# Performance work log

Hardware: AMD Instinct MI355X
Metric: run time of the kernel (lower is better)

The kernel has to match this reference:

```python
import jax, jax.numpy as jnp
import numpy as np

C_IN = 32
C_OUT = 32


def setup_inputs() -> dict:
    key = jax.random.key(0)
    k1, k2, k3 = jax.random.split(key, 3)
    B, N, P_DIM = 32, 4096, 64
    X = jax.random.normal(k1, (B, N, C_IN), dtype=jnp.float32)
    P = jax.random.normal(k2, (B, N, P_DIM), dtype=jnp.float32)
    # glorot-ish scale for the hypernetwork Dense kernel (p_dim -> c_in*c_out)
    scale = (2.0 / (P_DIM + C_IN * C_OUT)) ** 0.5
    Wk = jax.random.normal(k3, (P_DIM, C_IN * C_OUT), dtype=jnp.float32) * scale
    return {"X": X, "P": P, "Wk": Wk}


def reference(X, P, Wk):
    B, N, c_in = X.shape
    # hypernetwork: per-position weight generation  [B,N,p] @ [p, c_in*c_out]
    A = jnp.einsum('bnp,pq->bnq', P, Wk)
    W = A.reshape(B, N, c_in, C_OUT)          # [B,N,c_in,c_out]
    W = jax.nn.relu(W)                        # sigma(W)
    # batched per-position GEMV: y_bno = sum_i X_bni * W_bnio
    out = jnp.einsum('bni,bnio->bno', X, W)   # [B,N,c_out]
    return out
```

## Files before the change

kernel.cpp:

```cpp
#include <hip/hip_runtime.h>

#define CI 32
#define CO 32
#define PD 64
#define QDIM 1024
#define M_TOTAL (32*4096)
#define TILE_M 256
#define NBLK (M_TOTAL/TILE_M)
#define WG_THREADS 256

typedef float  f32x4  __attribute__((ext_vector_type(4)));
typedef float  f32x16 __attribute__((ext_vector_type(16)));
typedef __bf16 bf16x4 __attribute__((ext_vector_type(4)));
typedef __bf16 bf16x8 __attribute__((ext_vector_type(8)));

#define XLS 257
#define OLS 33

__global__ __launch_bounds__(256)
void wk_pack_kernel(const float* __restrict__ Wk, __bf16* __restrict__ wsF)
{
    __shared__ float tile[64][33];
    const int q0 = blockIdx.x * 32;
    const int t  = threadIdx.x;
#pragma unroll
    for (int s = 0; s < 2; ++s) {
        const int idx = t + s * 256;
        const int k = idx >> 3, ch = idx & 7;
        f32x4 v = *(const f32x4*)(Wk + (size_t)k * QDIM + q0 + ch * 4);
        tile[k][ch*4+0] = v[0]; tile[k][ch*4+1] = v[1];
        tile[k][ch*4+2] = v[2]; tile[k][ch*4+3] = v[3];
    }
    __syncthreads();
    const int qq = t >> 3;
    const int g  = t & 7;
    bf16x8 o;
#pragma unroll
    for (int j = 0; j < 8; ++j) o[j] = (__bf16)tile[g*8 + j][qq];
    *(bf16x8*)(wsF + (size_t)blockIdx.x * 2048 + g * 256 + qq * 8) = o;
}

__global__ __launch_bounds__(WG_THREADS, 2)
void cond_dense_kernel(const float* __restrict__ Xg, const float* __restrict__ Pg,
                       const __bf16* __restrict__ wsF, float* __restrict__ outg)
{
    __shared__ union {
        __bf16 p[TILE_M * PD];
        float  o[TILE_M * OLS];
    } U;
    __shared__ float Xl[CI * XLS];

    const int tid = threadIdx.x;
    const int l   = tid & 63;
    const int w   = tid >> 6;
    const int l31 = l & 31;
    const int hi  = l >> 5;
    const int mlo = w * 64 + l31;
    const int mhi = mlo + 32;
    const int tile0 = blockIdx.x * TILE_M;

    {
        const float* Pb = Pg + (size_t)tile0 * PD;
        const int pr = tid >> 4, pch = tid & 15;
#pragma unroll
        for (int s = 0; s < 16; ++s) {
            const int r = pr + s * 16;
            f32x4 v = *(const f32x4*)(Pb + (size_t)r * PD + pch * 4);
            bf16x4 bv;
#pragma unroll
            for (int j = 0; j < 4; ++j) bv[j] = (__bf16)v[j];
            char* dst = (char*)U.p + r * 128
                      + ((((pch >> 1) ^ (r & 7)) << 4) | ((pch & 1) * 8));
            *(bf16x4*)dst = bv;
        }
        const float* Xb = Xg + (size_t)tile0 * CI;
        const int xr = tid >> 3, xch = tid & 7;
#pragma unroll
        for (int s = 0; s < 8; ++s) {
            const int r = xr + s * 32;
            f32x4 v = *(const f32x4*)(Xb + (size_t)r * CI + xch * 4);
#pragma unroll
            for (int j = 0; j < 4; ++j)
                Xl[(xch * 4 + j) * XLS + r] = v[j];
        }
    }
    __syncthreads();

    bf16x8 bfA[4], bfB[4];
#pragma unroll
    for (int kq = 0; kq < 4; ++kq) {
        const int g = ((kq * 2 + hi) ^ (mlo & 7)) << 4;
        bfA[kq] = *(const bf16x8*)((const char*)U.p + mlo * 128 + g);
        bfB[kq] = *(const bf16x8*)((const char*)U.p + mhi * 128 + g);
    }

    f32x16 oA = {}, oB = {};
    const __bf16* abase = wsF + (size_t)hi * 256 + (size_t)l31 * 8;

    bf16x8 a0[4], a1[4];
    auto aload = [&](int i, bf16x8* buf) {
        const __bf16* ap = abase + (size_t)i * 2048;
        buf[0] = *(const bf16x8*)(ap);
        buf[1] = *(const bf16x8*)(ap +  512);
        buf[2] = *(const bf16x8*)(ap + 1024);
        buf[3] = *(const bf16x8*)(ap + 1536);
    };
    auto step = [&](const bf16x8* a, float xl, float xh) {
        f32x16 cA = {}, cB = {};
#pragma unroll
        for (int kq = 0; kq < 4; ++kq) {
            cA = __builtin_amdgcn_mfma_f32_32x32x16_bf16(a[kq], bfA[kq], cA, 0, 0, 0);
            cB = __builtin_amdgcn_mfma_f32_32x32x16_bf16(a[kq], bfB[kq], cB, 0, 0, 0);
        }
#pragma unroll
        for (int r = 0; r < 16; ++r) {
            oA[r] += fmaxf(cA[r], 0.0f) * xl;
            oB[r] += fmaxf(cB[r], 0.0f) * xh;
        }
    };

    aload(0, a0);
    aload(1, a1);
    for (int ii = 0; ii < 16; ++ii) {
        const int i0 = 2 * ii, i1 = i0 + 1;
        const float x0l = Xl[i0 * XLS + mlo], x0h = Xl[i0 * XLS + mhi];
        const float x1l = Xl[i1 * XLS + mlo], x1h = Xl[i1 * XLS + mhi];
        step(a0, x0l, x0h);
        if (ii < 15) aload(i0 + 2, a0);
        step(a1, x1l, x1h);
        if (ii < 15) aload(i1 + 2, a1);
    }

    __syncthreads();

#pragma unroll
    for (int r = 0; r < 16; ++r) {
        const int o = (r & 3) + 8 * (r >> 2) + 4 * hi;
        U.o[mlo * OLS + o] = oA[r];
        U.o[mhi * OLS + o] = oB[r];
    }
    __syncthreads();

    {
        const int sr = tid >> 3, sch = (tid & 7) * 4;
#pragma unroll
        for (int s = 0; s < 8; ++s) {
            const int r = sr + s * 32;
            f32x4 v;
#pragma unroll
            for (int j = 0; j < 4; ++j) v[j] = U.o[r * OLS + sch + j];
            *(f32x4*)(outg + (size_t)(tile0 + r) * CO + sch) = v;
        }
    }
}

extern "C" void kernel_launch(void* const* d_in, const int* in_sizes, int n_in,
                              void* d_out, int out_size, void* d_ws, size_t ws_size,
                              hipStream_t stream)
{
    const float* X  = (const float*)d_in[0];
    const float* P  = (const float*)d_in[1];
    const float* Wk = (const float*)d_in[2];
    float* out = (float*)d_out;
    __bf16* wsF = (__bf16*)d_ws;

    wk_pack_kernel<<<dim3(QDIM / 32), dim3(256), 0, stream>>>(Wk, wsF);
    cond_dense_kernel<<<dim3(NBLK), dim3(WG_THREADS), 0, stream>>>(X, P, wsF, out);
}
```

Baseline: 38.40 us.

## Stage packed hypernetwork weights through LDS with double-buffered async global_load_lds

Instead of every wave loading the packed bf16 Wk fragments straight from global memory into registers, each workgroup now cooperatively copies chunks of four input channels into a double-buffered LDS region using global_load_lds. The copy is reused by all four waves. The LDS buffer shares a union with the P tile and output staging, so an extra barrier is needed after the B fragments are read. This is meant to cut redundant global/L2 traffic and free registers, at the cost of a barrier per chunk and LDS read traffic.

```diff
diff --git a/kernel.cpp b/kernel.cpp
--- a/kernel.cpp
+++ b/kernel.cpp
@@ -8,6 +8,9 @@
 #define TILE_M 256
 #define NBLK (M_TOTAL/TILE_M)
 #define WG_THREADS 256
+#define CHUNK_I 4
+#define NCHUNK (CI/CHUNK_I)
+#define CHUNK_ELEMS (CHUNK_I*2048)
 
 typedef float  f32x4  __attribute__((ext_vector_type(4)));
 typedef float  f32x16 __attribute__((ext_vector_type(16)));
@@ -46,6 +49,7 @@
 {
     __shared__ union {
         __bf16 p[TILE_M * PD];
+        __bf16 a[2][CHUNK_ELEMS];
         float  o[TILE_M * OLS];
     } U;
     __shared__ float Xl[CI * XLS];
@@ -93,45 +97,54 @@
         bfA[kq] = *(const bf16x8*)((const char*)U.p + mlo * 128 + g);
         bfB[kq] = *(const bf16x8*)((const char*)U.p + mhi * 128 + g);
     }
+    __syncthreads();
+
+    auto stageA = [&](int c, int b) {
+        const __bf16* src = wsF + (size_t)c * CHUNK_ELEMS + tid * 8;
+        __bf16* dst = U.a[b] + tid * 8;
+#pragma unroll
+        for (int s = 0; s < 4; ++s)
+            __builtin_amdgcn_global_load_lds(
+                (const __attribute__((address_space(1))) void*)(src + s * 2048),
+                (__attribute__((address_space(3))) void*)(dst + s * 2048),
+                16, 0, 0);
+    };
 
     f32x16 oA = {}, oB = {};
-    const __bf16* abase = wsF + (size_t)hi * 256 + (size_t)l31 * 8;
 
-    bf16x8 a0[4], a1[4];
-    auto aload = [&](int i, bf16x8* buf) {
-        const __bf16* ap = abase + (size_t)i * 2048;
-        buf[0] = *(const bf16x8*)(ap);
-        buf[1] = *(const bf16x8*)(ap +  512);
-        buf[2] = *(const bf16x8*)(ap + 1024);
-        buf[3] = *(const bf16x8*)(ap + 1536);
-    };
-    auto step = [&](const bf16x8* a, float xl, float xh) {
-        f32x16 cA = {}, cB = {};
+    stageA(0, 0);
+    __syncthreads();
+
+    for (int c = 0; c < NCHUNK; ++c) {
+        if (c + 1 < NCHUNK) stageA(c + 1, (c + 1) & 1);
+        const __bf16* ab = U.a[c & 1];
 #pragma unroll
-        for (int kq = 0; kq < 4; ++kq) {
-            cA = __builtin_amdgcn_mfma_f32_32x32x16_bf16(a[kq], bfA[kq], cA, 0, 0, 0);
-            cB = __builtin_amdgcn_mfma_f32_32x32x16_bf16(a[kq], bfB[kq], cB, 0, 0, 0);
+        for (int il = 0; il < CHUNK_I; ++il) {
+            const int i = c * CHUNK_I + il;
+            const __bf16* ap = ab + il * 2048 + hi * 256 + l31 * 8;
+            bf16x8 a0 = *(const bf16x8*)(ap);
+            bf16x8 a1 = *(const bf16x8*)(ap +  512);
+            bf16x8 a2 = *(const bf16x8*)(ap + 1024);
+            bf16x8 a3 = *(const bf16x8*)(ap + 1536);
+            const float xl = Xl[i * XLS + mlo];
+            const float xh = Xl[i * XLS + mhi];
+            f32x16 cA = {}, cB = {};
+            cA = __builtin_amdgcn_mfma_f32_32x32x16_bf16(a0, bfA[0], cA, 0, 0, 0);
+            cB = __builtin_amdgcn_mfma_f32_32x32x16_bf16(a0, bfB[0], cB, 0, 0, 0);
+            cA = __builtin_amdgcn_mfma_f32_32x32x16_bf16(a1, bfA[1], cA, 0, 0, 0);
+            cB = __builtin_amdgcn_mfma_f32_32x32x16_bf16(a1, bfB[1], cB, 0, 0, 0);
+            cA = __builtin_amdgcn_mfma_f32_32x32x16_bf16(a2, bfA[2], cA, 0, 0, 0);
+            cB = __builtin_amdgcn_mfma_f32_32x32x16_bf16(a2, bfB[2], cB, 0, 0, 0);
+            cA = __builtin_amdgcn_mfma_f32_32x32x16_bf16(a3, bfA[3], cA, 0, 0, 0);
+            cB = __builtin_amdgcn_mfma_f32_32x32x16_bf16(a3, bfB[3], cB, 0, 0, 0);
+#pragma unroll
+            for (int r = 0; r < 16; ++r) {
+                oA[r] += fmaxf(cA[r], 0.0f) * xl;
+                oB[r] += fmaxf(cB[r], 0.0f) * xh;
+            }
         }
-#pragma unroll
-        for (int r = 0; r < 16; ++r) {
-            oA[r] += fmaxf(cA[r], 0.0f) * xl;
-            oB[r] += fmaxf(cB[r], 0.0f) * xh;
-        }
-    };
-
-    aload(0, a0);
-    aload(1, a1);
-    for (int ii = 0; ii < 16; ++ii) {
-        const int i0 = 2 * ii, i1 = i0 + 1;
-        const float x0l = Xl[i0 * XLS + mlo], x0h = Xl[i0 * XLS + mhi];
-        const float x1l = Xl[i1 * XLS + mlo], x1h = Xl[i1 * XLS + mhi];
-        step(a0, x0l, x0h);
-        if (ii < 15) aload(i0 + 2, a0);
-        step(a1, x1l, x1h);
-        if (ii < 15) aload(i1 + 2, a1);
+        __syncthreads();
     }
-
-    __syncthreads();
 
 #pragma unroll
     for (int r = 0; r < 16; ++r) {
```

Result: slower. 43.38 us (+13.0%).

## Shrink workgroups to one wave with 64-row tiles and direct output stores

Applied to the files above, without the earlier changes.

Each workgroup is cut from four waves over 256 rows to a single wave over 64 rows, giving four times as many blocks. All X and P global loads are issued up front into registers. The P and X staging reuse one shared-memory union, and outputs are written straight from the MFMA accumulators as f32x4 stores instead of going through shared memory. The aim is less shared memory per block, more resident waves and cheaper barriers. In exchange each block re-reads the packed weights on its own, so weight traffic per row goes up, and register pressure rises from the prefetched inputs.

```diff
diff --git a/kernel.cpp b/kernel.cpp
--- a/kernel.cpp
+++ b/kernel.cpp
@@ -5,17 +5,16 @@
 #define PD 64
 #define QDIM 1024
 #define M_TOTAL (32*4096)
-#define TILE_M 256
+#define TILE_M 64
 #define NBLK (M_TOTAL/TILE_M)
-#define WG_THREADS 256
+#define WG_THREADS 64
 
 typedef float  f32x4  __attribute__((ext_vector_type(4)));
 typedef float  f32x16 __attribute__((ext_vector_type(16)));
 typedef __bf16 bf16x4 __attribute__((ext_vector_type(4)));
 typedef __bf16 bf16x8 __attribute__((ext_vector_type(8)));
 
-#define XLS 257
-#define OLS 33
+#define XLS 65
 
 __global__ __launch_bounds__(256)
 void wk_pack_kernel(const float* __restrict__ Wk, __bf16* __restrict__ wsF)
@@ -40,59 +39,70 @@
     *(bf16x8*)(wsF + (size_t)blockIdx.x * 2048 + g * 256 + qq * 8) = o;
 }
 
-__global__ __launch_bounds__(WG_THREADS, 2)
+__global__ __launch_bounds__(WG_THREADS, 4)
 void cond_dense_kernel(const float* __restrict__ Xg, const float* __restrict__ Pg,
                        const __bf16* __restrict__ wsF, float* __restrict__ outg)
 {
     __shared__ union {
         __bf16 p[TILE_M * PD];
-        float  o[TILE_M * OLS];
+        float  x[CI * XLS];
     } U;
-    __shared__ float Xl[CI * XLS];
 
-    const int tid = threadIdx.x;
-    const int l   = tid & 63;
-    const int w   = tid >> 6;
+    const int l   = threadIdx.x;
     const int l31 = l & 31;
     const int hi  = l >> 5;
-    const int mlo = w * 64 + l31;
-    const int mhi = mlo + 32;
     const int tile0 = blockIdx.x * TILE_M;
 
+    f32x4 xr[8];
+    {
+        const float* Xb = Xg + (size_t)tile0 * CI;
+#pragma unroll
+        for (int s = 0; s < 8; ++s) {
+            const int id = l + 64 * s;
+            xr[s] = *(const f32x4*)(Xb + (size_t)(id >> 3) * CI + (id & 7) * 4);
+        }
+    }
+    f32x4 pr[16];
     {
         const float* Pb = Pg + (size_t)tile0 * PD;
-        const int pr = tid >> 4, pch = tid & 15;
 #pragma unroll
         for (int s = 0; s < 16; ++s) {
-            const int r = pr + s * 16;
-            f32x4 v = *(const f32x4*)(Pb + (size_t)r * PD + pch * 4);
-            bf16x4 bv;
+            const int id = l + 64 * s;
+            pr[s] = *(const f32x4*)(Pb + (size_t)(id >> 4) * PD + (id & 15) * 4);
+        }
+    }
+
 #pragma unroll
-            for (int j = 0; j < 4; ++j) bv[j] = (__bf16)v[j];
-            char* dst = (char*)U.p + r * 128
-                      + ((((pch >> 1) ^ (r & 7)) << 4) | ((pch & 1) * 8));
-            *(bf16x4*)dst = bv;
-        }
-        const float* Xb = Xg + (size_t)tile0 * CI;
-        const int xr = tid >> 3, xch = tid & 7;
+    for (int s = 0; s < 16; ++s) {
+        const int id = l + 64 * s;
+        const int r = id >> 4, ch = id & 15;
+        bf16x4 bv;
 #pragma unroll
-        for (int s = 0; s < 8; ++s) {
-            const int r = xr + s * 32;
-            f32x4 v = *(const f32x4*)(Xb + (size_t)r * CI + xch * 4);
-#pragma unroll
-            for (int j = 0; j < 4; ++j)
-                Xl[(xch * 4 + j) * XLS + r] = v[j];
-        }
+        for (int j = 0; j < 4; ++j) bv[j] = (__bf16)pr[s][j];
+        char* dst = (char*)U.p + r * 128
+                  + ((((ch >> 1) ^ (r & 7)) << 4) | ((ch & 1) * 8));
+        *(bf16x4*)dst = bv;
     }
     __syncthreads();
 
     bf16x8 bfA[4], bfB[4];
 #pragma unroll
     for (int kq = 0; kq < 4; ++kq) {
-        const int g = ((kq * 2 + hi) ^ (mlo & 7)) << 4;
-        bfA[kq] = *(const bf16x8*)((const char*)U.p + mlo * 128 + g);
-        bfB[kq] = *(const bf16x8*)((const char*)U.p + mhi * 128 + g);
+        const int g = ((kq * 2 + hi) ^ (l31 & 7)) << 4;
+        bfA[kq] = *(const bf16x8*)((const char*)U.p + l31 * 128 + g);
+        bfB[kq] = *(const bf16x8*)((const char*)U.p + (l31 + 32) * 128 + g);
     }
+    __syncthreads();
+
+#pragma unroll
+    for (int s = 0; s < 8; ++s) {
+        const int id = l + 64 * s;
+        const int r = id >> 3, c = (id & 7) * 4;
+#pragma unroll
+        for (int j = 0; j < 4; ++j)
+            U.x[(c + j) * XLS + r] = xr[s][j];
+    }
+    __syncthreads();
 
     f32x16 oA = {}, oB = {};
     const __bf16* abase = wsF + (size_t)hi * 256 + (size_t)l31 * 8;
@@ -105,7 +115,9 @@
         buf[2] = *(const bf16x8*)(ap + 1024);
         buf[3] = *(const bf16x8*)(ap + 1536);
     };
-    auto step = [&](const bf16x8* a, float xl, float xh) {
+    auto step = [&](const bf16x8* a, int i) {
+        const float xl = U.x[i * XLS + l31];
+        const float xh = U.x[i * XLS + l31 + 32];
         f32x16 cA = {}, cB = {};
 #pragma unroll
         for (int kq = 0; kq < 4; ++kq) {
@@ -122,34 +134,22 @@
     aload(0, a0);
     aload(1, a1);
     for (int ii = 0; ii < 16; ++ii) {
-        const int i0 = 2 * ii, i1 = i0 + 1;
-        const float x0l = Xl[i0 * XLS + mlo], x0h = Xl[i0 * XLS + mhi];
-        const float x1l = Xl[i1 * XLS + mlo], x1h = Xl[i1 * XLS + mhi];
-        step(a0, x0l, x0h);
-        if (ii < 15) aload(i0 + 2, a0);
-        step(a1, x1l, x1h);
-        if (ii < 15) aload(i1 + 2, a1);
+        step(a0, 2 * ii);
+        if (ii < 15) aload(2 * ii + 2, a0);
+        step(a1, 2 * ii + 1);
+        if (ii < 15) aload(2 * ii + 3, a1);
     }
 
-    __syncthreads();
-
+    {
+        float* orow = outg + (size_t)(tile0 + l31) * CO + 4 * hi;
+        float* orow2 = orow + 32 * CO;
 #pragma unroll
-    for (int r = 0; r < 16; ++r) {
-        const int o = (r & 3) + 8 * (r >> 2) + 4 * hi;
-        U.o[mlo * OLS + o] = oA[r];
-        U.o[mhi * OLS + o] = oB[r];
-    }
-    __syncthreads();
-
-    {
-        const int sr = tid >> 3, sch = (tid & 7) * 4;
+        for (int rq = 0; rq < 4; ++rq) {
+            f32x4 vA, vB;
 #pragma unroll
-        for (int s = 0; s < 8; ++s) {
-            const int r = sr + s * 32;
-            f32x4 v;
-#pragma unroll
-            for (int j = 0; j < 4; ++j) v[j] = U.o[r * OLS + sch + j];
-            *(f32x4*)(outg + (size_t)(tile0 + r) * CO + sch) = v;
+            for (int j = 0; j < 4; ++j) { vA[j] = oA[4*rq + j]; vB[j] = oB[4*rq + j]; }
+            *(f32x4*)(orow  + 8 * rq) = vA;
+            *(f32x4*)(orow2 + 8 * rq) = vB;
         }
     }
 }
```

Measured after the change: 76.67 us. 2x slower.
